# Performance work log

Measured on AMD Instinct MI355X. Metric: run time of the kernel, lower is better.

The kernel has to match this reference:

```python
import jax, jax.numpy as jnp
import numpy as np

B = 2048          # number of local graphs
L = 63            # local_edge_num -> 64 nodes per graph
N = B * (L + 1)   # 131072 total nodes
F = 32            # num_features
E = 524288        # random edges
C = 64            # gat hidden dim
A = 16            # action_dim
NEG_SLOPE = 0.2


def _gat(x, src, dst, W, a_src, a_dst, b, heads, out):
    """PyG-style GATConv (concat=True): gather -> leaky-relu logits ->
    per-destination segment softmax -> weighted scatter-sum."""
    n = x.shape[0]
    h = (x @ W).reshape(n, heads, out)                  # [N,H,C]
    al_s = jnp.sum(h * a_src, axis=-1)                  # [N,H]
    al_d = jnp.sum(h * a_dst, axis=-1)                  # [N,H]
    e = jax.nn.leaky_relu(al_s[src] + al_d[dst], NEG_SLOPE)  # [E,H]
    m = jax.ops.segment_max(e, dst, num_segments=n)
    e = jnp.exp(e - m[dst])
    s = jax.ops.segment_sum(e, dst, num_segments=n)
    alpha = e / (s[dst] + 1e-16)                        # [E,H]
    msg = h[src] * alpha[:, :, None]                    # [E,H,C]  dominant traffic
    agg = jax.ops.segment_sum(msg, dst, num_segments=n)
    return agg.reshape(n, heads * out) + b


def setup_inputs() -> dict:
    key = jax.random.key(0)
    ks = jax.random.split(key, 24)
    node_features = jax.random.normal(ks[0], (N, F), dtype=jnp.float32)
    edge_index = jax.random.randint(ks[1], (2, E), 0, N, dtype=jnp.int32)

    def p(k, shape, scale=0.1):
        return jax.random.normal(k, shape, dtype=jnp.float32) * scale

    return {
        "node_features": node_features,
        "edge_index": edge_index,
        # gat1: F -> 64, heads=4
        "W1": p(ks[2], (F, 4 * C)), "a1s": p(ks[3], (4, C)), "a1d": p(ks[4], (4, C)), "b1": jnp.zeros((4 * C,), jnp.float32),
        # gat2: 256 -> 64, heads=1
        "W2": p(ks[5], (4 * C, C)), "a2s": p(ks[6], (1, C)), "a2d": p(ks[7], (1, C)), "b2": jnp.zeros((C,), jnp.float32),
        # gat3: 64 -> 64, heads=1
        "W3": p(ks[8], (C, C)), "a3s": p(ks[9], (1, C)), "a3d": p(ks[10], (1, C)), "b3": jnp.zeros((C,), jnp.float32),
        # actor MLP
        "fcW1": p(ks[11], (C * (L + 1), 64)), "fcb1": jnp.zeros((64,), jnp.float32),
        "fcW2": p(ks[12], (64, 32)), "fcb2": jnp.zeros((32,), jnp.float32),
        "fcW3": p(ks[13], (32, A)), "fcb3": jnp.zeros((A,), jnp.float32),
    }


def reference(node_features, edge_index,
              W1, a1s, a1d, b1, W2, a2s, a2d, b2, W3, a3s, a3d, b3,
              fcW1, fcb1, fcW2, fcb2, fcW3, fcb3):
    n = node_features.shape[0]
    loops = jnp.arange(n, dtype=edge_index.dtype)       # GATConv add_self_loops=True
    src = jnp.concatenate([edge_index[0], loops])
    dst = jnp.concatenate([edge_index[1], loops])

    x = jax.nn.relu(_gat(node_features, src, dst, W1, a1s, a1d, b1, 4, C))
    x = jax.nn.relu(_gat(x, src, dst, W2, a2s, a2d, b2, 1, C))
    x = jax.nn.relu(_gat(x, src, dst, W3, a3s, a3d, b3, 1, C))

    x_gat = x.reshape(-1, C * (L + 1))                  # [B, 64*(L+1)]
    h = jax.nn.relu(x_gat @ fcW1 + fcb1)
    h = jax.nn.relu(h @ fcW2 + fcb2)
    action_mean = jax.nn.softmax(h @ fcW3 + fcb3, axis=-1)  # [B, A]
    return action_mean
```

## Files before the change

### kernel.cpp

```cpp
#include <hip/hip_runtime.h>
#include <math.h>

#define NN 131072
#define FF 32
#define EE 524288
#define ET (EE + NN)
#define BB 2048

__global__ void init_counts(int* counts) {
  int i = blockIdx.x * 256 + threadIdx.x;
  counts[i] = 1;
}

__global__ void count_edges(const int* __restrict__ ei, int* counts) {
  int e = blockIdx.x * 256 + threadIdx.x;
  atomicAdd(&counts[ei[EE + e]], 1);
}

__global__ void scan_block(const int* __restrict__ counts, int* offs, int* blksums) {
  __shared__ int sd[256];
  int t = threadIdx.x;
  int i = blockIdx.x * 256 + t;
  int v = counts[i];
  sd[t] = v;
  __syncthreads();
  for (int o = 1; o < 256; o <<= 1) {
    int x = (t >= o) ? sd[t - o] : 0;
    __syncthreads();
    sd[t] += x;
    __syncthreads();
  }
  offs[i] = sd[t] - v;
  if (t == 255) blksums[blockIdx.x] = sd[255];
}

__global__ void scan_sums(int* blksums) {
  __shared__ int sd[512];
  int t = threadIdx.x;
  int v = blksums[t];
  sd[t] = v;
  __syncthreads();
  for (int o = 1; o < 512; o <<= 1) {
    int x = (t >= o) ? sd[t - o] : 0;
    __syncthreads();
    sd[t] += x;
    __syncthreads();
  }
  blksums[t] = sd[t] - v;
}

__global__ void scan_add(int* offs, int* cursor, const int* __restrict__ blksums) {
  int i = blockIdx.x * 256 + threadIdx.x;
  int o = offs[i] + blksums[blockIdx.x];
  offs[i] = o;
  cursor[i] = o;
  if (i == 0) offs[NN] = ET;
}

__global__ void fill_csr(const int* __restrict__ ei, int* cursor,
                         int* esrc, int* edst) {
  int i = blockIdx.x * 256 + threadIdx.x;
  int s, d;
  if (i < EE) { s = ei[i]; d = ei[EE + i]; }
  else        { s = d = i - EE; }
  int pos = atomicAdd(&cursor[d], 1);
  esrc[pos] = s;
  edst[pos] = d;
}

__global__ void l1_avec(const float* __restrict__ W1, const float* __restrict__ a1s,
                        const float* __restrict__ a1d, float* __restrict__ wts,
                        float* __restrict__ wtd) {
  int t = threadIdx.x;
  int h = t >> 5, k = t & 31;
  float as = 0.f, ad = 0.f;
  #pragma unroll
  for (int c = 0; c < 64; ++c) {
    float w = W1[k * 256 + h * 64 + c];
    as += w * a1s[h * 64 + c];
    ad += w * a1d[h * 64 + c];
  }
  wts[t] = as;
  wtd[t] = ad;
}

__global__ __launch_bounds__(256) void l1_logits(
    const float* __restrict__ x, const float* __restrict__ wts,
    const float* __restrict__ wtd, float* __restrict__ als, float* __restrict__ ald) {
  __shared__ float sx[64 * 33];
  __shared__ float sts[128], std_[128];
  int t = threadIdx.x;
  int n0 = blockIdx.x * 64;
  #pragma unroll
  for (int j = 0; j < 8; ++j) {
    int idx = t + j * 256;
    sx[(idx >> 5) * 33 + (idx & 31)] = x[(size_t)n0 * 32 + idx];
  }
  if (t < 128) sts[t] = wts[t]; else std_[t - 128] = wtd[t - 128];
  __syncthreads();
  int nl = t >> 2, h = t & 3;
  float vs = 0.f, vd = 0.f;
  #pragma unroll
  for (int k = 0; k < 32; ++k) {
    float xv = sx[nl * 33 + k];
    vs += xv * sts[h * 32 + k];
    vd += xv * std_[h * 32 + k];
  }
  als[(n0 + nl) * 4 + h] = vs;
  ald[(n0 + nl) * 4 + h] = vd;
}

__global__ void edge_w4(const int* __restrict__ esrc, const int* __restrict__ edst,
                        const float* __restrict__ als, const float* __restrict__ ald,
                        float4* __restrict__ w4) {
  int j = blockIdx.x * 256 + threadIdx.x;
  int s = esrc[j], d = edst[j];
  float4 a = ((const float4*)als)[s];
  float4 b = ((const float4*)ald)[d];
  float e0 = a.x + b.x; e0 = (e0 > 0.f) ? e0 : 0.2f * e0;
  float e1 = a.y + b.y; e1 = (e1 > 0.f) ? e1 : 0.2f * e1;
  float e2 = a.z + b.z; e2 = (e2 > 0.f) ? e2 : 0.2f * e2;
  float e3 = a.w + b.w; e3 = (e3 > 0.f) ? e3 : 0.2f * e3;
  w4[j] = make_float4(__expf(e0), __expf(e1), __expf(e2), __expf(e3));
}

__global__ void edge_w1(const int* __restrict__ esrc, const int* __restrict__ edst,
                        const float* __restrict__ als, const float* __restrict__ ald,
                        float* __restrict__ w) {
  int j = blockIdx.x * 256 + threadIdx.x;
  float e = als[esrc[j]] + ald[edst[j]];
  e = (e > 0.f) ? e : 0.2f * e;
  w[j] = __expf(e);
}

__global__ __launch_bounds__(256) void gat1_agg(
    const float* __restrict__ x, const int* __restrict__ offs,
    const int* __restrict__ esrc, const float4* __restrict__ w4arr,
    float* __restrict__ ya) {
  int t = threadIdx.x;
  int wv = t >> 6, lane = t & 63;
  int k = lane & 31, jp = lane >> 5;
  int n = blockIdx.x * 4 + wv;
  int start = offs[n], end = offs[n + 1];
  float xa0 = 0.f, xa1 = 0.f, xa2 = 0.f, xa3 = 0.f;
  float S0 = 0.f, S1 = 0.f, S2 = 0.f, S3 = 0.f;
  int j = start + jp;
  for (; j + 2 < end; j += 4) {
    int sA_ = esrc[j], sB_ = esrc[j + 2];
    float4 wA = w4arr[j], wB = w4arr[j + 2];
    float xA = x[(size_t)sA_ * 32 + k];
    float xB = x[(size_t)sB_ * 32 + k];
    xa0 += wA.x * xA; xa1 += wA.y * xA; xa2 += wA.z * xA; xa3 += wA.w * xA;
    S0 += wA.x; S1 += wA.y; S2 += wA.z; S3 += wA.w;
    xa0 += wB.x * xB; xa1 += wB.y * xB; xa2 += wB.z * xB; xa3 += wB.w * xB;
    S0 += wB.x; S1 += wB.y; S2 += wB.z; S3 += wB.w;
  }
  if (j < end) {
    int s = esrc[j];
    float4 w = w4arr[j];
    float xv = x[(size_t)s * 32 + k];
    xa0 += w.x * xv; xa1 += w.y * xv; xa2 += w.z * xv; xa3 += w.w * xv;
    S0 += w.x; S1 += w.y; S2 += w.z; S3 += w.w;
  }
  xa0 += __shfl_xor(xa0, 32); S0 += __shfl_xor(S0, 32);
  xa1 += __shfl_xor(xa1, 32); S1 += __shfl_xor(S1, 32);
  xa2 += __shfl_xor(xa2, 32); S2 += __shfl_xor(S2, 32);
  xa3 += __shfl_xor(xa3, 32); S3 += __shfl_xor(S3, 32);
  if (jp == 0) {
    ya[(size_t)n * 128 +  0 + k] = xa0 / (S0 + 1e-16f);
    ya[(size_t)n * 128 + 32 + k] = xa1 / (S1 + 1e-16f);
  } else {
    ya[(size_t)n * 128 + 64 + k] = xa2 / (S2 + 1e-16f);
    ya[(size_t)n * 128 + 96 + k] = xa3 / (S3 + 1e-16f);
  }
}

__global__ __launch_bounds__(256) void gemm1_bd(
    const float* __restrict__ ya, const float* __restrict__ W1,
    const float* __restrict__ b1, float* __restrict__ agg1) {
  __shared__ float sW1[32 * 256];
  __shared__ float sA[32 * 144];
  int t = threadIdx.x;
  int row0 = blockIdx.x * 32;
  #pragma unroll
  for (int j = 0; j < 8; ++j) {
    int li4 = t + j * 256;
    *(float4*)&sW1[li4 * 4] = *(const float4*)&W1[li4 * 4];
  }
  #pragma unroll
  for (int j = 0; j < 4; ++j) {
    int li = t + j * 256;
    int r = li >> 5, f4 = li & 31;
    int hh = f4 >> 3, kk4 = (f4 & 7) * 4;
    *(float4*)&sA[r * 144 + hh * 36 + kk4] =
        *(const float4*)&ya[(size_t)(row0 + r) * 128 + f4 * 4];
  }
  __syncthreads();
  int cq = t & 63;
  int rs = t >> 6;
  int hh = cq >> 4;
  float4 acc[8];
  #pragma unroll
  for (int rp = 0; rp < 8; ++rp) acc[rp] = make_float4(0.f, 0.f, 0.f, 0.f);
  #pragma unroll
  for (int kk = 0; kk < 32; ++kk) {
    float4 w4 = *(const float4*)&sW1[kk * 256 + cq * 4];
    #pragma unroll
    for (int rp = 0; rp < 8; ++rp) {
      float a = sA[(rs * 8 + rp) * 144 + hh * 36 + kk];
      acc[rp].x += a * w4.x; acc[rp].y += a * w4.y;
      acc[rp].z += a * w4.z; acc[rp].w += a * w4.w;
    }
  }
  float4 b4 = *(const float4*)&b1[cq * 4];
  #pragma unroll
  for (int rp = 0; rp < 8; ++rp) {
    int r = row0 + rs * 8 + rp;
    float4 v = acc[rp];
    v.x = fmaxf(v.x + b4.x, 0.f); v.y = fmaxf(v.y + b4.y, 0.f);
    v.z = fmaxf(v.z + b4.z, 0.f); v.w = fmaxf(v.w + b4.w, 0.f);
    *(float4*)&agg1[(size_t)r * 256 + cq * 4] = v;
  }
}

template <int KTILES, int ROWS, bool AL>
__global__ __launch_bounds__(256) void gemm_n64(
    const float* __restrict__ A, const float* __restrict__ W,
    const float* __restrict__ bias, const float* __restrict__ a_s,
    const float* __restrict__ a_d, float* __restrict__ out,
    float* __restrict__ als, float* __restrict__ ald) {
  constexpr int K = KTILES * 64;
  constexpr int RPT = ROWS / 16;
  constexpr int SAS = 68;
  __shared__ float sW[64 * 64];
  __shared__ float sA[ROWS * SAS];
  int t = threadIdx.x;
  int cq = t & 15;
  int rs = t >> 4;
  int row0 = blockIdx.x * ROWS;
  float4 acc[RPT];
  #pragma unroll
  for (int rp = 0; rp < RPT; ++rp) acc[rp] = make_float4(0.f, 0.f, 0.f, 0.f);
  for (int kt = 0; kt < KTILES; ++kt) {
    #pragma unroll
    for (int j = 0; j < 4; ++j) {
      int li = t + j * 256;
      int kk = li >> 4, cc = (li & 15) * 4;
      *(float4*)&sW[kk * 64 + cc] =
          *(const float4*)&W[(size_t)(kt * 64 + kk) * 64 + cc];
    }
    #pragma unroll
    for (int j = 0; j < ROWS / 16; ++j) {
      int li = t + j * 256;
      int r = li >> 4, kkq = (li & 15) * 4;
      *(float4*)&sA[r * SAS + kkq] =
          *(const float4*)&A[(size_t)(row0 + r) * K + kt * 64 + kkq];
    }
    __syncthreads();
    #pragma unroll
    for (int kq = 0; kq < 16; ++kq) {
      float4 a4[RPT];
      #pragma unroll
      for (int rp = 0; rp < RPT; ++rp)
        a4[rp] = *(const float4*)&sA[(rs * RPT + rp) * SAS + kq * 4];
      #pragma unroll
      for (int i = 0; i < 4; ++i) {
        float4 w4 = *(const float4*)&sW[(kq * 4 + i) * 64 + cq * 4];
        #pragma unroll
        for (int rp = 0; rp < RPT; ++rp) {
          float a = (i == 0) ? a4[rp].x : (i == 1) ? a4[rp].y
                  : (i == 2) ? a4[rp].z : a4[rp].w;
          acc[rp].x += a * w4.x; acc[rp].y += a * w4.y;
          acc[rp].z += a * w4.z; acc[rp].w += a * w4.w;
        }
      }
    }
    __syncthreads();
  }
  #pragma unroll
  for (int rp = 0; rp < RPT; ++rp) {
    int r = row0 + rs * RPT + rp;
    if constexpr (AL) {
      *(float4*)&out[(size_t)r * 64 + cq * 4] = acc[rp];
      float4 s4 = *(const float4*)&a_s[cq * 4];
      float4 d4 = *(const float4*)&a_d[cq * 4];
      float vs = acc[rp].x * s4.x + acc[rp].y * s4.y + acc[rp].z * s4.z + acc[rp].w * s4.w;
      float vd = acc[rp].x * d4.x + acc[rp].y * d4.y + acc[rp].z * d4.z + acc[rp].w * d4.w;
      #pragma unroll
      for (int o = 8; o >= 1; o >>= 1) { vs += __shfl_xor(vs, o); vd += __shfl_xor(vd, o); }
      if (cq == 0) { als[r] = vs; ald[r] = vd; }
    } else {
      float4 b4 = *(const float4*)&bias[cq * 4];
      float4 v = acc[rp];
      v.x = fmaxf(v.x + b4.x, 0.f); v.y = fmaxf(v.y + b4.y, 0.f);
      v.z = fmaxf(v.z + b4.z, 0.f); v.w = fmaxf(v.w + b4.w, 0.f);
      *(float4*)&out[(size_t)r * 64 + cq * 4] = v;
    }
  }
}

__global__ __launch_bounds__(256) void gat_aggregate(
    const float* __restrict__ hsrc, const float* __restrict__ warr,
    const int* __restrict__ offs, const int* __restrict__ esrc,
    const float* __restrict__ bias, float* __restrict__ out) {
  int wv = threadIdx.x >> 6;
  int lane = threadIdx.x & 63;
  int n = blockIdx.x * 4 + wv;
  int start = offs[n], end = offs[n + 1];
  float acc = 0.f, S = 0.f;
  int j = start;
  for (; j + 4 <= end; j += 4) {
    int s0 = esrc[j], s1 = esrc[j+1], s2 = esrc[j+2], s3 = esrc[j+3];
    float w0 = warr[j], w1 = warr[j+1], w2 = warr[j+2], w3 = warr[j+3];
    float v0 = hsrc[(size_t)s0 * 64 + lane];
    float v1 = hsrc[(size_t)s1 * 64 + lane];
    float v2 = hsrc[(size_t)s2 * 64 + lane];
    float v3 = hsrc[(size_t)s3 * 64 + lane];
    acc += w0 * v0; acc += w1 * v1; acc += w2 * v2; acc += w3 * v3;
    S += w0 + w1 + w2 + w3;
  }
  for (; j < end; ++j) {
    int s = esrc[j]; float w = warr[j];
    acc += w * hsrc[(size_t)s * 64 + lane];
    S += w;
  }
  float v = acc / (S + 1e-16f) + bias[lane];
  out[(size_t)n * 64 + lane] = fmaxf(v, 0.f);
}

__global__ __launch_bounds__(256) void fc23_softmax(
    const float* __restrict__ h1, const float* __restrict__ W2,
    const float* __restrict__ b2, const float* __restrict__ W3,
    const float* __restrict__ b3, float* __restrict__ out) {
  int ws = threadIdx.x >> 6;
  int row = blockIdx.x * 4 + ws;
  int lane = threadIdx.x & 63;
  __shared__ float sh2[4][32];
  if (lane < 32) {
    float acc = b2[lane];
    for (int k = 0; k < 64; ++k) acc += h1[row * 64 + k] * W2[k * 32 + lane];
    sh2[ws][lane] = fmaxf(acc, 0.f);
  }
  __syncthreads();
  float logit = -INFINITY;
  if (lane < 16) {
    float acc = b3[lane];
    for (int k = 0; k < 32; ++k) acc += sh2[ws][k] * W3[k * 16 + lane];
    logit = acc;
  }
  float mx = logit;
  #pragma unroll
  for (int o = 8; o >= 1; o >>= 1) mx = fmaxf(mx, __shfl_xor(mx, o));
  float ex = (lane < 16) ? __expf(logit - mx) : 0.f;
  float ssum = ex;
  #pragma unroll
  for (int o = 8; o >= 1; o >>= 1) ssum += __shfl_xor(ssum, o);
  if (lane < 16) out[row * 16 + lane] = ex / ssum;
}

extern "C" void kernel_launch(void* const* d_in, const int* in_sizes, int n_in,
                              void* d_out, int out_size, void* d_ws, size_t ws_size,
                              hipStream_t stream) {
  const float* x0   = (const float*)d_in[0];
  const int*   ei   = (const int*)d_in[1];
  const float* W1   = (const float*)d_in[2];
  const float* a1s  = (const float*)d_in[3];
  const float* a1d  = (const float*)d_in[4];
  const float* b1   = (const float*)d_in[5];
  const float* W2   = (const float*)d_in[6];
  const float* a2s  = (const float*)d_in[7];
  const float* a2d  = (const float*)d_in[8];
  const float* b2   = (const float*)d_in[9];
  const float* W3   = (const float*)d_in[10];
  const float* a3s  = (const float*)d_in[11];
  const float* a3d  = (const float*)d_in[12];
  const float* b3   = (const float*)d_in[13];
  const float* fcW1 = (const float*)d_in[14];
  const float* fcb1 = (const float*)d_in[15];
  const float* fcW2 = (const float*)d_in[16];
  const float* fcb2 = (const float*)d_in[17];
  const float* fcW3 = (const float*)d_in[18];
  const float* fcb3 = (const float*)d_in[19];
  float* out = (float*)d_out;

  float* agg1   = (float*)d_ws;
  float* h23    = agg1 + (size_t)NN * 256;
  float* agg23  = h23 + (size_t)NN * 64;
  float* als1   = agg23 + (size_t)NN * 64;
  float* ald1   = als1 + (size_t)NN * 4;
  float* als2   = ald1 + (size_t)NN * 4;
  float* ald2   = als2 + NN;
  float* wts    = ald2 + NN;
  float* wtd    = wts + 128;
  int*   counts = (int*)(wtd + 128);
  int*   offs   = counts + NN;
  int*   cursor = offs + NN + 1;
  int*   esrc   = cursor + NN;
  int*   edst   = esrc + ET;
  int*   blksums= edst + ET;
  float4* w41   = (float4*)agg1;
  float* ya     = h23;
  float* als3   = agg1;
  float* ald3   = agg1 + NN;
  float* hfc1   = agg1 + 2 * (size_t)NN;
  float* w2     = agg1 + 4 * (size_t)NN;
  float* w3arr  = w2 + ET;

  init_counts<<<NN / 256, 256, 0, stream>>>(counts);
  count_edges<<<EE / 256, 256, 0, stream>>>(ei, counts);
  scan_block<<<NN / 256, 256, 0, stream>>>(counts, offs, blksums);
  scan_sums<<<1, 512, 0, stream>>>(blksums);
  scan_add<<<NN / 256, 256, 0, stream>>>(offs, cursor, blksums);
  fill_csr<<<ET / 256, 256, 0, stream>>>(ei, cursor, esrc, edst);

  l1_avec<<<1, 128, 0, stream>>>(W1, a1s, a1d, wts, wtd);
  l1_logits<<<NN / 64, 256, 0, stream>>>(x0, wts, wtd, als1, ald1);
  edge_w4<<<ET / 256, 256, 0, stream>>>(esrc, edst, als1, ald1, w41);
  gat1_agg<<<NN / 4, 256, 0, stream>>>(x0, offs, esrc, w41, ya);
  gemm1_bd<<<NN / 32, 256, 0, stream>>>(ya, W1, b1, agg1);
  gemm_n64<4, 32, true><<<NN / 32, 256, 0, stream>>>(agg1, W2, nullptr, a2s, a2d, h23, als2, ald2);
  edge_w1<<<ET / 256, 256, 0, stream>>>(esrc, edst, als2, ald2, w2);
  gat_aggregate<<<NN / 4, 256, 0, stream>>>(h23, w2, offs, esrc, b2, agg23);
  gemm_n64<1, 32, true><<<NN / 32, 256, 0, stream>>>(agg23, W3, nullptr, a3s, a3d, h23, als3, ald3);
  edge_w1<<<ET / 256, 256, 0, stream>>>(esrc, edst, als3, ald3, w3arr);
  gat_aggregate<<<NN / 4, 256, 0, stream>>>(h23, w3arr, offs, esrc, b3, agg23);
  gemm_n64<64, 16, false><<<BB / 16, 256, 0, stream>>>(agg23, fcW1, fcb1, nullptr, nullptr, hfc1, nullptr, nullptr);
  fc23_softmax<<<BB / 4, 256, 0, stream>>>(hfc1, fcW2, fcb2, fcW3, fcb3, out);
}
```

Before: 577.1 us.

## Split-K the actor FC1 GEMM and fuse partial reduction into FC2/softmax

Replaces the 128-block FC1 GEMM with a split-K kernel using 32 K-slices, launching 4096 blocks that each write a partial 16x64 tile. The partials, the bias and the ReLU are summed inside the fc23_softmax kernel, and FC2 now reads its input from shared memory. This targets the low parallelism of the original FC1 launch. In exchange it adds extra partial-sum traffic and repeated reads of the weight tiles. It also drops a block barrier and relies on per-wave shared-memory ordering.

```diff
diff --git a/kernel.cpp b/kernel.cpp
--- a/kernel.cpp
+++ b/kernel.cpp
@@ -6,6 +6,7 @@
 #define EE 524288
 #define ET (EE + NN)
 #define BB 2048
+#define KSPLIT 32
 
 __global__ void init_counts(int* counts) {
   int i = blockIdx.x * 256 + threadIdx.x;
@@ -297,6 +298,46 @@
       *(float4*)&out[(size_t)r * 64 + cq * 4] = v;
     }
   }
+}
+
+__global__ __launch_bounds__(256) void gemm_fc1_split(
+    const float* __restrict__ A, const float* __restrict__ W,
+    float* __restrict__ part) {
+  __shared__ float sW[128 * 64];
+  __shared__ float sA[16 * 132];
+  int t = threadIdx.x;
+  int bid = blockIdx.x;
+  int rt = bid >> 5;
+  int sp = bid & 31;
+  #pragma unroll
+  for (int j = 0; j < 8; ++j) {
+    int li = t + j * 256;
+    int kk = li >> 4, cc = (li & 15) * 4;
+    *(float4*)&sW[kk * 64 + cc] =
+        *(const float4*)&W[(size_t)(sp * 128 + kk) * 64 + cc];
+  }
+  #pragma unroll
+  for (int j = 0; j < 2; ++j) {
+    int li = t + j * 256;
+    int r = li >> 5, kq4 = (li & 31) * 4;
+    *(float4*)&sA[r * 132 + kq4] =
+        *(const float4*)&A[(size_t)(rt * 16 + r) * 4096 + sp * 128 + kq4];
+  }
+  __syncthreads();
+  int cq = t & 15;
+  int rs = t >> 4;
+  float4 acc = make_float4(0.f, 0.f, 0.f, 0.f);
+  #pragma unroll
+  for (int kq = 0; kq < 32; ++kq) {
+    float4 a4 = *(const float4*)&sA[rs * 132 + kq * 4];
+    #pragma unroll
+    for (int i = 0; i < 4; ++i) {
+      float4 w4 = *(const float4*)&sW[(kq * 4 + i) * 64 + cq * 4];
+      float a = (i == 0) ? a4.x : (i == 1) ? a4.y : (i == 2) ? a4.z : a4.w;
+      acc.x += a * w4.x; acc.y += a * w4.y; acc.z += a * w4.z; acc.w += a * w4.w;
+    }
+  }
+  *(float4*)&part[((size_t)sp * BB + rt * 16 + rs) * 64 + cq * 4] = acc;
 }
 
 __global__ __launch_bounds__(256) void gat_aggregate(
@@ -329,22 +370,35 @@
 }
 
 __global__ __launch_bounds__(256) void fc23_softmax(
-    const float* __restrict__ h1, const float* __restrict__ W2,
-    const float* __restrict__ b2, const float* __restrict__ W3,
-    const float* __restrict__ b3, float* __restrict__ out) {
+    const float* __restrict__ part, const float* __restrict__ fcb1,
+    const float* __restrict__ W2, const float* __restrict__ b2,
+    const float* __restrict__ W3, const float* __restrict__ b3,
+    float* __restrict__ out) {
   int ws = threadIdx.x >> 6;
   int row = blockIdx.x * 4 + ws;
   int lane = threadIdx.x & 63;
+  __shared__ float sh1[4][64];
   __shared__ float sh2[4][32];
+  float h1 = fcb1[lane];
+  #pragma unroll
+  for (int sp = 0; sp < KSPLIT; sp += 4) {
+    float p0 = part[((size_t)(sp + 0) * BB + row) * 64 + lane];
+    float p1 = part[((size_t)(sp + 1) * BB + row) * 64 + lane];
+    float p2 = part[((size_t)(sp + 2) * BB + row) * 64 + lane];
+    float p3 = part[((size_t)(sp + 3) * BB + row) * 64 + lane];
+    h1 += p0 + p1 + p2 + p3;
+  }
+  sh1[ws][lane] = fmaxf(h1, 0.f);
   if (lane < 32) {
     float acc = b2[lane];
-    for (int k = 0; k < 64; ++k) acc += h1[row * 64 + k] * W2[k * 32 + lane];
+    #pragma unroll
+    for (int k = 0; k < 64; ++k) acc += sh1[ws][k] * W2[k * 32 + lane];
     sh2[ws][lane] = fmaxf(acc, 0.f);
   }
-  __syncthreads();
   float logit = -INFINITY;
   if (lane < 16) {
     float acc = b3[lane];
+    #pragma unroll
     for (int k = 0; k < 32; ++k) acc += sh2[ws][k] * W3[k * 16 + lane];
     logit = acc;
   }
@@ -402,9 +456,9 @@
   float* ya     = h23;
   float* als3   = agg1;
   float* ald3   = agg1 + NN;
-  float* hfc1   = agg1 + 2 * (size_t)NN;
-  float* w2     = agg1 + 4 * (size_t)NN;
+  float* w2     = agg1 + 2 * (size_t)NN;
   float* w3arr  = w2 + ET;
+  float* part   = w3arr + ET;
 
   init_counts<<<NN / 256, 256, 0, stream>>>(counts);
   count_edges<<<EE / 256, 256, 0, stream>>>(ei, counts);
@@ -424,6 +478,6 @@
   gemm_n64<1, 32, true><<<NN / 32, 256, 0, stream>>>(agg23, W3, nullptr, a3s, a3d, h23, als3, ald3);
   edge_w1<<<ET / 256, 256, 0, stream>>>(esrc, edst, als3, ald3, w3arr);
   gat_aggregate<<<NN / 4, 256, 0, stream>>>(h23, w3arr, offs, esrc, b3, agg23);
-  gemm_n64<64, 16, false><<<BB / 16, 256, 0, stream>>>(agg23, fcW1, fcb1, nullptr, nullptr, hfc1, nullptr, nullptr);
-  fc23_softmax<<<BB / 4, 256, 0, stream>>>(hfc1, fcW2, fcb2, fcW3, fcb3, out);
-}
+  gemm_fc1_split<<<128 * KSPLIT, 256, 0, stream>>>(agg23, fcW1, part);
+  fc23_softmax<<<BB / 4, 256, 0, stream>>>(part, fcb1, fcW2, fcb2, fcW3, fcb3, out);
+}
```

Result: faster. 514.2 us (-10.9%).
